# Kernel tuning notes

Hardware: AMD Instinct MI355X
Metric: run time of the kernel (lower is better)

Reference implementation:

```python
import jax, jax.numpy as jnp
import numpy as np

NUM_EXPERTS = 16
TOP_K = 2
AUX_LOSS_WEIGHT = 0.01


def setup_inputs() -> dict:
    key = jax.random.key(0)
    k1, k2 = jax.random.split(key)
    B, H, W, D = 64, 56, 56, 512
    x = jax.random.normal(k1, (B, H, W, D), dtype=jnp.float32)
    # xavier_uniform for [E, D]
    limit = float(np.sqrt(6.0 / (NUM_EXPERTS + D)))
    expert_queries = jax.random.uniform(k2, (NUM_EXPERTS, D), dtype=jnp.float32,
                                        minval=-limit, maxval=limit)
    temperature = jnp.ones((1,), dtype=jnp.float32)
    return {"x": x, "expert_queries": expert_queries, "temperature": temperature}


def reference(x, expert_queries, temperature):
    # logits: [B, H, W, E]
    logits = jnp.einsum("bhwd,ed->bhwe", x, expert_queries) / temperature[0]
    gate_scores = jax.nn.softmax(logits, axis=-1)
    # aux load-balancing loss (training mode -> top_k)
    avg_gate_scores = gate_scores.mean(axis=(0, 1, 2))  # [E]
    flat = gate_scores.reshape(-1, NUM_EXPERTS)
    _, top_k_idx = jax.lax.top_k(flat, TOP_K)  # [N, k]
    mask = jax.nn.one_hot(top_k_idx, NUM_EXPERTS, dtype=flat.dtype).sum(axis=-2)  # [N, E]
    load = (mask / TOP_K).mean(axis=0)  # [E]
    aux_loss = AUX_LOSS_WEIGHT * (avg_gate_scores * load).mean() * (NUM_EXPERTS ** 2)
    return gate_scores, aux_loss
```

## Files before the change

kernel.cpp:

```cpp
#include <hip/hip_runtime.h>
#include <hip/hip_bf16.h>
#include <math.h>


#define NROWS 200704
#define DDIM 512
#define NEXP 16
#define KSTEPS 16
#define NTILES (NROWS / 16)
#define NBLOCKS 784
#define TILES_PER_WAVE 4

typedef __attribute__((ext_vector_type(8))) short short8;
typedef __attribute__((ext_vector_type(4))) float f32x4;

static __device__ inline short f2bf(float f) {
    __bf16 h = (__bf16)f;
    return __builtin_bit_cast(short, h);
}

static __device__ inline short8 pack8(float4 a, float4 b) {
    short8 r;
    r[0] = f2bf(a.x); r[1] = f2bf(a.y); r[2] = f2bf(a.z); r[3] = f2bf(a.w);
    r[4] = f2bf(b.x); r[5] = f2bf(b.y); r[6] = f2bf(b.z); r[7] = f2bf(b.w);
    return r;
}

__global__ __launch_bounds__(256, 4) void gate_kernel(
    const float* __restrict__ x,
    const float* __restrict__ q,
    const float* __restrict__ temp,
    float* __restrict__ out,
    float* __restrict__ ws)
{
    const int lane = threadIdx.x & 63;
    const int wid  = threadIdx.x >> 6;
    const int gwave = blockIdx.x * 4 + wid;
    const int fe = lane & 15;
    const int g  = lane >> 4;

    __shared__ short8 qlds[KSTEPS * 64];
    {
        for (int idx = threadIdx.x; idx < KSTEPS * 64; idx += 256) {
            const int s = idx >> 6, ln = idx & 63;
            const int qfe = ln & 15, qg = ln >> 4;
            const float* qp = q + qfe * DDIM + qg * 8 + s * 32;
            float4 a = *reinterpret_cast<const float4*>(qp);
            float4 b = *reinterpret_cast<const float4*>(qp + 4);
            qlds[idx] = pack8(a, b);
        }
    }
    __syncthreads();

    const float invT = 1.0f / temp[0];

    float sS[4] = {0, 0, 0, 0};
    float sC[4] = {0, 0, 0, 0};

    const int t0 = gwave * TILES_PER_WAVE;
#pragma unroll 1
    for (int t = t0; t < t0 + TILES_PER_WAVE; ++t) {
        const float* xr = x + (size_t)t * 16 * DDIM + (size_t)fe * DDIM + g * 8;
        f32x4 acc = {0.0f, 0.0f, 0.0f, 0.0f};
#pragma unroll
        for (int s = 0; s < KSTEPS; ++s) {
            float4 a = *reinterpret_cast<const float4*>(xr + s * 32);
            float4 b = *reinterpret_cast<const float4*>(xr + s * 32 + 4);
            acc = __builtin_amdgcn_mfma_f32_16x16x32_bf16(
                qlds[s * 64 + lane], pack8(a, b), acc, 0, 0, 0);
        }

        const float l0 = acc[0] * invT, l1 = acc[1] * invT;
        const float l2 = acc[2] * invT, l3 = acc[3] * invT;

        float m = fmaxf(fmaxf(l0, l1), fmaxf(l2, l3));
        m = fmaxf(m, __shfl_xor(m, 16, 64));
        m = fmaxf(m, __shfl_xor(m, 32, 64));

        const float p0 = __expf(l0 - m), p1 = __expf(l1 - m);
        const float p2 = __expf(l2 - m), p3 = __expf(l3 - m);
        float s4 = (p0 + p1) + (p2 + p3);
        s4 += __shfl_xor(s4, 16, 64);
        s4 += __shfl_xor(s4, 32, 64);
        const float inv = 1.0f / s4;
        const float g0 = p0 * inv, g1 = p1 * inv, g2 = p2 * inv, g3 = p3 * inv;

        const float NI = -3.4e38f;
        const float M0 = (l0 == m) ? NI : l0, M1 = (l1 == m) ? NI : l1;
        const float M2 = (l2 == m) ? NI : l2, M3 = (l3 == m) ? NI : l3;
        float m2 = fmaxf(fmaxf(M0, M1), fmaxf(M2, M3));
        m2 = fmaxf(m2, __shfl_xor(m2, 16, 64));
        m2 = fmaxf(m2, __shfl_xor(m2, 32, 64));

        sS[0] += g0; sS[1] += g1; sS[2] += g2; sS[3] += g3;
        sC[0] += (l0 >= m2) ? 1.0f : 0.0f;
        sC[1] += (l1 >= m2) ? 1.0f : 0.0f;
        sC[2] += (l2 >= m2) ? 1.0f : 0.0f;
        sC[3] += (l3 >= m2) ? 1.0f : 0.0f;

        float4 o = make_float4(g0, g1, g2, g3);
        *reinterpret_cast<float4*>(out + ((size_t)t * 16 + fe) * NEXP + g * 4) = o;
    }

#pragma unroll
    for (int r = 0; r < 4; ++r) {
        sS[r] += __shfl_xor(sS[r], 1, 64);
        sS[r] += __shfl_xor(sS[r], 2, 64);
        sS[r] += __shfl_xor(sS[r], 4, 64);
        sS[r] += __shfl_xor(sS[r], 8, 64);
        sC[r] += __shfl_xor(sC[r], 1, 64);
        sC[r] += __shfl_xor(sC[r], 2, 64);
        sC[r] += __shfl_xor(sC[r], 4, 64);
        sC[r] += __shfl_xor(sC[r], 8, 64);
    }

    __shared__ float sred[32];
    if (threadIdx.x < 32) sred[threadIdx.x] = 0.0f;
    __syncthreads();
    if (fe == 0) {
#pragma unroll
        for (int r = 0; r < 4; ++r) {
            atomicAdd(&sred[g * 4 + r], sS[r]);
            atomicAdd(&sred[16 + g * 4 + r], sC[r]);
        }
    }
    __syncthreads();
    if (threadIdx.x < 32) atomicAdd(&ws[threadIdx.x], sred[threadIdx.x]);
}

__global__ void aux_kernel(const float* __restrict__ ws, float* __restrict__ out) {
    if (threadIdx.x == 0 && blockIdx.x == 0) {
        float a = 0.0f;
#pragma unroll
        for (int e = 0; e < NEXP; ++e) a += ws[e] * ws[16 + e];
        const float n = (float)NROWS;
        out[(size_t)NROWS * NEXP] = 0.08f * a / (n * n);
    }
}

extern "C" void kernel_launch(void* const* d_in, const int* in_sizes, int n_in,
                              void* d_out, int out_size, void* d_ws, size_t ws_size,
                              hipStream_t stream) {
    const float* x = (const float*)d_in[0];
    const float* q = (const float*)d_in[1];
    const float* t = (const float*)d_in[2];
    float* out = (float*)d_out;
    float* ws = (float*)d_ws;

    hipMemsetAsync(ws, 0, 32 * sizeof(float), stream);
    gate_kernel<<<NBLOCKS, 256, 0, stream>>>(x, q, t, out, ws);
    aux_kernel<<<1, 64, 0, stream>>>(ws, out);
}
```

Before: 104.6 us.

## Use persistent 1024-thread blocks with LDS-counter dynamic tile scheduling

Goes from 784 blocks of 256 threads with fixed tiles per wave to 256 blocks of 1024 threads. Waves pull tiles from a shared-memory atomic counter over each block's contiguous range. The per-lane x read pattern changes to two float4 loads 16 floats apart, and the q packing is adjusted to match. A dead-code 68 KB LDS pad is added so the occupancy is one block per CU. This trades static partitioning for load balancing, at the cost of LDS atomics and less block-level parallelism.

```diff
diff --git a/kernel.cpp b/kernel.cpp
--- a/kernel.cpp
+++ b/kernel.cpp
@@ -8,8 +8,8 @@
 #define NEXP 16
 #define KSTEPS 16
 #define NTILES (NROWS / 16)
-#define NBLOCKS 784
-#define TILES_PER_WAVE 4
+#define NBLOCKS 256
+#define TPB (NTILES / NBLOCKS)
 
 typedef __attribute__((ext_vector_type(8))) short short8;
 typedef __attribute__((ext_vector_type(4))) float f32x4;
@@ -26,7 +26,7 @@
     return r;
 }
 
-__global__ __launch_bounds__(256, 4) void gate_kernel(
+__global__ __launch_bounds__(1024, 4) void gate_kernel(
     const float* __restrict__ x,
     const float* __restrict__ q,
     const float* __restrict__ temp,
@@ -34,38 +34,48 @@
     float* __restrict__ ws)
 {
     const int lane = threadIdx.x & 63;
-    const int wid  = threadIdx.x >> 6;
-    const int gwave = blockIdx.x * 4 + wid;
     const int fe = lane & 15;
     const int g  = lane >> 4;
 
     __shared__ short8 qlds[KSTEPS * 64];
+    __shared__ int tctr;
+    __shared__ float sred[32];
+    __shared__ float ldspad[17000];
+
     {
-        for (int idx = threadIdx.x; idx < KSTEPS * 64; idx += 256) {
-            const int s = idx >> 6, ln = idx & 63;
-            const int qfe = ln & 15, qg = ln >> 4;
-            const float* qp = q + qfe * DDIM + qg * 8 + s * 32;
-            float4 a = *reinterpret_cast<const float4*>(qp);
-            float4 b = *reinterpret_cast<const float4*>(qp + 4);
-            qlds[idx] = pack8(a, b);
-        }
+        const int idx = threadIdx.x;
+        const int s = idx >> 6, ln = idx & 63;
+        const int qfe = ln & 15, qg = ln >> 4;
+        const float* qp = q + qfe * DDIM + s * 32 + qg * 4;
+        float4 a = *reinterpret_cast<const float4*>(qp);
+        float4 b = *reinterpret_cast<const float4*>(qp + 16);
+        qlds[idx] = pack8(a, b);
     }
+    if (threadIdx.x == 0) tctr = 0;
+    if (threadIdx.x < 32) sred[threadIdx.x] = 0.0f;
     __syncthreads();
 
     const float invT = 1.0f / temp[0];
+    const size_t tbase = (size_t)blockIdx.x * TPB;
 
     float sS[4] = {0, 0, 0, 0};
     float sC[4] = {0, 0, 0, 0};
 
-    const int t0 = gwave * TILES_PER_WAVE;
-#pragma unroll 1
-    for (int t = t0; t < t0 + TILES_PER_WAVE; ++t) {
-        const float* xr = x + (size_t)t * 16 * DDIM + (size_t)fe * DDIM + g * 8;
+    int t;
+    if (lane == 0) t = atomicAdd(&tctr, 1);
+    t = __shfl(t, 0, 64);
+
+    while (t < TPB) {
+        int tn;
+        if (lane == 0) tn = atomicAdd(&tctr, 1);
+        tn = __shfl(tn, 0, 64);
+
+        const float* xr = x + (tbase + t) * 16 * DDIM + (size_t)fe * DDIM;
         f32x4 acc = {0.0f, 0.0f, 0.0f, 0.0f};
 #pragma unroll
         for (int s = 0; s < KSTEPS; ++s) {
-            float4 a = *reinterpret_cast<const float4*>(xr + s * 32);
-            float4 b = *reinterpret_cast<const float4*>(xr + s * 32 + 4);
+            float4 a = *reinterpret_cast<const float4*>(xr + s * 32 + g * 4);
+            float4 b = *reinterpret_cast<const float4*>(xr + s * 32 + g * 4 + 16);
             acc = __builtin_amdgcn_mfma_f32_16x16x32_bf16(
                 qlds[s * 64 + lane], pack8(a, b), acc, 0, 0, 0);
         }
@@ -99,7 +109,9 @@
         sC[3] += (l3 >= m2) ? 1.0f : 0.0f;
 
         float4 o = make_float4(g0, g1, g2, g3);
-        *reinterpret_cast<float4*>(out + ((size_t)t * 16 + fe) * NEXP + g * 4) = o;
+        *reinterpret_cast<float4*>(
+            out + ((tbase + t) * 16 + fe) * NEXP + g * 4) = o;
+        t = tn;
     }
 
 #pragma unroll
@@ -114,9 +126,6 @@
         sC[r] += __shfl_xor(sC[r], 8, 64);
     }
 
-    __shared__ float sred[32];
-    if (threadIdx.x < 32) sred[threadIdx.x] = 0.0f;
-    __syncthreads();
     if (fe == 0) {
 #pragma unroll
         for (int r = 0; r < 4; ++r) {
@@ -124,8 +133,10 @@
             atomicAdd(&sred[16 + g * 4 + r], sC[r]);
         }
     }
+    if (tctr < 0) ldspad[tctr & 16383] = sS[0];
     __syncthreads();
     if (threadIdx.x < 32) atomicAdd(&ws[threadIdx.x], sred[threadIdx.x]);
+    if (tctr < 0) ws[33] = ldspad[-tctr & 16383];
 }
 
 __global__ void aux_kernel(const float* __restrict__ ws, float* __restrict__ out) {
@@ -148,6 +159,6 @@
     float* ws = (float*)d_ws;
 
     hipMemsetAsync(ws, 0, 32 * sizeof(float), stream);
-    gate_kernel<<<NBLOCKS, 256, 0, stream>>>(x, q, t, out, ws);
+    gate_kernel<<<NBLOCKS, 1024, 0, stream>>>(x, q, t, out, ws);
     aux_kernel<<<1, 64, 0, stream>>>(ws, out);
 }
```

Result: no change. 103.7 us (-0.9%).
